# Kernel optimization log

Measured on AMD Instinct MI355X. Metric: run time of the kernel, lower is better.

Reference implementation:

```python
import jax, jax.numpy as jnp
import numpy as np

HEAD = 8
D = 128
GIN = 256
GOUT = 256
N = 50000
E = 800000


def gt_layer(edge_index, embeds, qT, kT, vT, ln_s, ln_b):
    rows, cols = edge_index[0], edge_index[1]
    n, d = embeds.shape
    hd = d // HEAD
    rowE = embeds[rows]  # [E, d]
    colE = embeds[cols]  # [E, d]
    q = (rowE @ qT).reshape(-1, HEAD, hd)
    k = (colE @ kT).reshape(-1, HEAD, hd)
    v = (colE @ vT).reshape(-1, HEAD, hd)
    att = jnp.clip(jnp.einsum('ehd,ehd->eh', q, k), -10.0, 10.0)
    expAtt = jnp.exp(att)  # [E, H]
    attNorm = jax.ops.segment_sum(expAtt, rows, num_segments=n)[rows]  # scatter-softmax denom
    att = expAtt / (attNorm + 1e-8)
    res = (att[..., None] * v).reshape(-1, d)  # [E, d]
    agg = jax.ops.segment_sum(res, rows, num_segments=n)  # [n, d]
    out = agg + embeds
    mu = jnp.mean(out, axis=-1, keepdims=True)
    var = jnp.mean((out - mu) ** 2, axis=-1, keepdims=True)
    return (out - mu) / jnp.sqrt(var + 1e-6) * ln_s + ln_b


def setup_inputs() -> dict:
    key = jax.random.key(0)
    ks = jax.random.split(key, 16)
    def xavier(k, shape):
        lim = np.sqrt(6.0 / (shape[0] + shape[1]))
        return jax.random.uniform(k, shape, jnp.float32, -lim, lim)
    inp = {
        'x': jax.random.normal(ks[0], (N, GIN), jnp.float32),
        'edge_index': jax.random.randint(ks[1], (2, E), 0, N, jnp.int64),
        'W_P_w': xavier(ks[2], (GIN, D)),
        'W_P_b': jnp.zeros((D,), jnp.float32),
        'W_pos': jax.random.uniform(ks[3], (1, D), jnp.float32, -0.02, 0.02),
        'q1': xavier(ks[4], (D, D)), 'k1': xavier(ks[5], (D, D)), 'v1': xavier(ks[6], (D, D)),
        'ln1_s': jnp.ones((D,), jnp.float32), 'ln1_b': jnp.zeros((D,), jnp.float32),
        'q2': xavier(ks[7], (D, D)), 'k2': xavier(ks[8], (D, D)), 'v2': xavier(ks[9], (D, D)),
        'ln2_s': jnp.ones((D,), jnp.float32), 'ln2_b': jnp.zeros((D,), jnp.float32),
        'inv_w': xavier(ks[10], (D, GOUT)),
        'inv_b': jnp.zeros((GOUT,), jnp.float32),
    }
    return inp


def reference(x, edge_index, W_P_w, W_P_b, W_pos, q1, k1, v1, ln1_s, ln1_b,
              q2, k2, v2, ln2_s, ln2_b, inv_w, inv_b):
    z = x @ W_P_w + W_P_b          # W_P linear: [N, D]
    embeds = z + W_pos              # if_pos; dropout is identity in eval
    embeds = gt_layer(edge_index, embeds, q1, k1, v1, ln1_s, ln1_b)
    embeds = gt_layer(edge_index, embeds, q2, k2, v2, ln2_s, ln2_b)
    return embeds @ inv_w + inv_b   # [N, GOUT]
```

## Files before the change

### kernel.cpp

```cpp
#include <hip/hip_runtime.h>
#include <hip/hip_bf16.h>

#define HEADS 8
#define DIM 128

typedef short s8v __attribute__((ext_vector_type(8)));
typedef float f4v __attribute__((ext_vector_type(4)));

__device__ __forceinline__ float bf2f(unsigned int lo16) {
    union { unsigned int i; float f; } v; v.i = lo16 << 16; return v.f;
}
__device__ __forceinline__ unsigned short f2bf(float f) {
    __hip_bfloat16 h = __float2bfloat16(f);
    return *reinterpret_cast<unsigned short*>(&h);
}
__device__ __forceinline__ int imin(int a, int b) { return a < b ? a : b; }

__global__ void detect_width_k(const unsigned int* __restrict__ w, int* __restrict__ flag) {
    __shared__ int cnt;
    if (threadIdx.x == 0) cnt = 0;
    __syncthreads();
    if (w[2 * threadIdx.x + 1] == 0u) atomicAdd(&cnt, 1);
    __syncthreads();
    if (threadIdx.x == 0) flag[0] = (cnt > 192) ? 1 : 0;
}

__global__ void cvt_edges_k(const void* __restrict__ ei, const int* __restrict__ flag,
                            int n2, int* __restrict__ out) {
    int i = blockIdx.x * 256 + threadIdx.x;
    if (i < n2) {
        if (flag[0])
            out[i] = (int)((const long long*)ei)[i];
        else
            out[i] = ((const int*)ei)[i];
    }
}

__global__ void count_deg_k(const int* __restrict__ rows, int E, int* __restrict__ deg) {
    int e = blockIdx.x * 256 + threadIdx.x;
    if (e < E) atomicAdd(&deg[rows[e]], 1);
}

__global__ void scan1_k(const int* __restrict__ deg, int n,
                        int* __restrict__ incl, int* __restrict__ blkSums) {
    __shared__ int s[256];
    int i = blockIdx.x * 256 + threadIdx.x;
    int v = (i < n) ? deg[i] : 0;
    s[threadIdx.x] = v;
    __syncthreads();
    for (int off = 1; off < 256; off <<= 1) {
        int t = (threadIdx.x >= off) ? s[threadIdx.x - off] : 0;
        __syncthreads();
        s[threadIdx.x] += t;
        __syncthreads();
    }
    if (i < n) incl[i] = s[threadIdx.x];
    if (threadIdx.x == 255) blkSums[blockIdx.x] = s[255];
}

__global__ void scan2_k(int* __restrict__ blkSums, int nb) {
    __shared__ int s[256];
    int v = (threadIdx.x < nb) ? blkSums[threadIdx.x] : 0;
    s[threadIdx.x] = v;
    __syncthreads();
    for (int off = 1; off < 256; off <<= 1) {
        int t = (threadIdx.x >= off) ? s[threadIdx.x - off] : 0;
        __syncthreads();
        s[threadIdx.x] += t;
        __syncthreads();
    }
    if (threadIdx.x < nb) blkSums[threadIdx.x] = s[threadIdx.x] - v;
}

__global__ void scan3_k(const int* __restrict__ incl, const int* __restrict__ deg,
                        const int* __restrict__ blkOff, int n,
                        int* __restrict__ rowPtr, int* __restrict__ cursor) {
    int i = blockIdx.x * 256 + threadIdx.x;
    if (i < n) {
        int inc = incl[i] + blkOff[blockIdx.x];
        rowPtr[i + 1] = inc;
        cursor[i] = inc - deg[i];
    }
    if (i == 0) rowPtr[0] = 0;
}

__global__ void scatter_k(const int* __restrict__ rows, const int* __restrict__ cols, int E,
                          int* __restrict__ cursor, int* __restrict__ colIdx) {
    int e = blockIdx.x * 256 + threadIdx.x;
    if (e < E) {
        int pos = atomicAdd(&cursor[rows[e]], 1);
        colIdx[pos] = cols[e];
    }
}

__global__ void build_wfrag_k(const float* __restrict__ W, unsigned short* __restrict__ dst,
                              int Kd, int Nd, int split, int ncomp) {
    int f = blockIdx.x * 256 + threadIdx.x;
    int KS = Kd >> 5;
    int perPhase = (Nd / 16 / split) * KS * 64;
    int total = ncomp * split * perPhase;
    if (f >= total) return;
    int comp = f / (split * perPhase);
    int r1 = f - comp * split * perPhase;
    int p = r1 / perPhase;
    int r = r1 - p * perPhase;
    int nt = r / (KS * 64);
    int r2 = r - nt * KS * 64;
    int ks = r2 >> 6, lane = r2 & 63;
    int n = p * (Nd / split) + nt * 16 + (lane & 15);
    int k0 = ks * 32 + (lane >> 4) * 8;
    unsigned short tmp[8];
#pragma unroll
    for (int j = 0; j < 8; j++) {
        float w = W[(size_t)(k0 + j) * Nd + n];
        unsigned short hi = f2bf(w);
        tmp[j] = (comp == 0) ? hi : f2bf(w - bf2f(hi));
    }
#pragma unroll
    for (int j = 0; j < 8; j++) dst[(size_t)f * 8 + j] = tmp[j];
}

__global__ __launch_bounds__(512) void proj_k(
    const float* __restrict__ A, const unsigned short* __restrict__ wfrag,
    const float* __restrict__ b0, const float* __restrict__ b1,
    unsigned short* __restrict__ ehi, unsigned short* __restrict__ elo, int M)
{
    constexpr int KD = 256, KS = 8, NTp = 4;
    constexpr int FRp = NTp * KS * 64;
    __shared__ s8v lds[2 * FRp];

    const int tid = threadIdx.x;
    const int lane = tid & 63;
    const int m16 = lane & 15, q4 = lane >> 4;
    const int phase = blockIdx.y;
    const int pairIdx = blockIdx.x * 8 + (tid >> 6);
    const int nPairs = (M + 31) >> 5;

    for (int idx = tid; idx < 2 * FRp; idx += 512) {
        int comp = idx / FRp, r = idx - comp * FRp;
        lds[idx] = *(const s8v*)(wfrag + ((size_t)((comp * 2 + phase) * FRp) + r) * 8);
    }
    __syncthreads();
    if (pairIdx >= nPairs) return;

    const int row0 = pairIdx * 32;
    const int rA0 = imin(row0 + m16, M - 1);
    const int rA1 = imin(row0 + 16 + m16, M - 1);

    f4v acc0[NTp], acc1[NTp];
#pragma unroll
    for (int nt = 0; nt < NTp; nt++) { acc0[nt] = (f4v){0,0,0,0}; acc1[nt] = (f4v){0,0,0,0}; }

    for (int ks = 0; ks < KS; ks++) {
        const float* pa0 = A + (size_t)rA0 * KD + ks * 32 + q4 * 8;
        const float* pa1 = A + (size_t)rA1 * KD + ks * 32 + q4 * 8;
        s8v a0h, a0l, a1h, a1l;
#pragma unroll
        for (int j = 0; j < 8; j++) {
            float x0 = pa0[j], x1 = pa1[j];
            unsigned short h0 = f2bf(x0), h1 = f2bf(x1);
            a0h[j] = (short)h0; a1h[j] = (short)h1;
            a0l[j] = (short)f2bf(x0 - bf2f(h0));
            a1l[j] = (short)f2bf(x1 - bf2f(h1));
        }
#pragma unroll
        for (int nt = 0; nt < NTp; nt++) {
            s8v bh = lds[0 * FRp + (nt * KS + ks) * 64 + lane];
            s8v bl = lds[1 * FRp + (nt * KS + ks) * 64 + lane];
            acc0[nt] = __builtin_amdgcn_mfma_f32_16x16x32_bf16(a0h, bh, acc0[nt], 0, 0, 0);
            acc0[nt] = __builtin_amdgcn_mfma_f32_16x16x32_bf16(a0h, bl, acc0[nt], 0, 0, 0);
            acc0[nt] = __builtin_amdgcn_mfma_f32_16x16x32_bf16(a0l, bh, acc0[nt], 0, 0, 0);
            acc1[nt] = __builtin_amdgcn_mfma_f32_16x16x32_bf16(a1h, bh, acc1[nt], 0, 0, 0);
            acc1[nt] = __builtin_amdgcn_mfma_f32_16x16x32_bf16(a1h, bl, acc1[nt], 0, 0, 0);
            acc1[nt] = __builtin_amdgcn_mfma_f32_16x16x32_bf16(a1l, bh, acc1[nt], 0, 0, 0);
        }
    }

#pragma unroll
    for (int nt = 0; nt < NTp; nt++) {
        const int col = phase * 64 + nt * 16 + m16;
        const float bias = b0[col] + b1[col];
#pragma unroll
        for (int r = 0; r < 4; r++) {
            const int gr0 = row0 + q4 * 4 + r;
            if (gr0 < M) {
                float v = acc0[nt][r] + bias;
                unsigned short h = f2bf(v);
                ehi[(size_t)gr0 * DIM + col] = h;
                elo[(size_t)gr0 * DIM + col] = f2bf(v - bf2f(h));
            }
            const int gr1 = gr0 + 16;
            if (gr1 < M && row0 + 16 < M) {
                float v = acc1[nt][r] + bias;
                unsigned short h = f2bf(v);
                ehi[(size_t)gr1 * DIM + col] = h;
                elo[(size_t)gr1 * DIM + col] = f2bf(v - bf2f(h));
            }
        }
    }
}

__global__ __launch_bounds__(512) void qkv_k(
    const unsigned short* __restrict__ ehi, const unsigned short* __restrict__ elo,
    const unsigned short* __restrict__ wfrag,
    float* __restrict__ Qb, unsigned short* __restrict__ KVb, int M)
{
    constexpr int KS = 4, NTp = 4;
    constexpr int FRp = NTp * KS * 64;
    constexpr int MATFR = 4 * FRp;
    __shared__ s8v lds[5 * FRp];

    const int tid = threadIdx.x;
    const int lane = tid & 63;
    const int m16 = lane & 15, q4 = lane >> 4;
    const int phase = blockIdx.y;
    const int pairIdx = blockIdx.x * 8 + (tid >> 6);
    const int nPairs = (M + 31) >> 5;

    for (int idx = tid; idx < 5 * FRp; idx += 512) {
        int s = idx / FRp, r = idx - s * FRp;
        int mat = (s < 2) ? 0 : (s < 4) ? 1 : 2;
        int comp = (s < 4) ? (s & 1) : 0;
        lds[idx] = *(const s8v*)(wfrag + ((size_t)mat * MATFR + (comp * 2 + phase) * FRp + r) * 8);
    }
    __syncthreads();
    if (pairIdx >= nPairs) return;

    const int row0 = pairIdx * 32;
    const int rA0 = imin(row0 + m16, M - 1);
    const int rA1 = imin(row0 + 16 + m16, M - 1);

    s8v a0h[KS], a0l[KS], a1h[KS], a1l[KS];
#pragma unroll
    for (int ks = 0; ks < KS; ks++) {
        a0h[ks] = *(const s8v*)(ehi + (size_t)rA0 * DIM + ks * 32 + q4 * 8);
        a0l[ks] = *(const s8v*)(elo + (size_t)rA0 * DIM + ks * 32 + q4 * 8);
        a1h[ks] = *(const s8v*)(ehi + (size_t)rA1 * DIM + ks * 32 + q4 * 8);
        a1l[ks] = *(const s8v*)(elo + (size_t)rA1 * DIM + ks * 32 + q4 * 8);
    }

    f4v aQ0[NTp], aQ1[NTp], aK0[NTp], aK1[NTp], aV0[NTp], aV1[NTp];
#pragma unroll
    for (int nt = 0; nt < NTp; nt++) {
        aQ0[nt] = (f4v){0,0,0,0}; aQ1[nt] = (f4v){0,0,0,0};
        aK0[nt] = (f4v){0,0,0,0}; aK1[nt] = (f4v){0,0,0,0};
        aV0[nt] = (f4v){0,0,0,0}; aV1[nt] = (f4v){0,0,0,0};
    }

#pragma unroll
    for (int ks = 0; ks < KS; ks++) {
#pragma unroll
        for (int nt = 0; nt < NTp; nt++) {
            const int fi = (nt * KS + ks) * 64 + lane;
            s8v qh = lds[0 * FRp + fi], ql = lds[1 * FRp + fi];
            s8v kh = lds[2 * FRp + fi], kl = lds[3 * FRp + fi];
            s8v vh = lds[4 * FRp + fi];
            aQ0[nt] = __builtin_amdgcn_mfma_f32_16x16x32_bf16(a0h[ks], qh, aQ0[nt], 0, 0, 0);
            aQ0[nt] = __builtin_amdgcn_mfma_f32_16x16x32_bf16(a0h[ks], ql, aQ0[nt], 0, 0, 0);
            aQ0[nt] = __builtin_amdgcn_mfma_f32_16x16x32_bf16(a0l[ks], qh, aQ0[nt], 0, 0, 0);
            aQ1[nt] = __builtin_amdgcn_mfma_f32_16x16x32_bf16(a1h[ks], qh, aQ1[nt], 0, 0, 0);
            aQ1[nt] = __builtin_amdgcn_mfma_f32_16x16x32_bf16(a1h[ks], ql, aQ1[nt], 0, 0, 0);
            aQ1[nt] = __builtin_amdgcn_mfma_f32_16x16x32_bf16(a1l[ks], qh, aQ1[nt], 0, 0, 0);
            aK0[nt] = __builtin_amdgcn_mfma_f32_16x16x32_bf16(a0h[ks], kh, aK0[nt], 0, 0, 0);
            aK0[nt] = __builtin_amdgcn_mfma_f32_16x16x32_bf16(a0h[ks], kl, aK0[nt], 0, 0, 0);
            aK0[nt] = __builtin_amdgcn_mfma_f32_16x16x32_bf16(a0l[ks], kh, aK0[nt], 0, 0, 0);
            aK1[nt] = __builtin_amdgcn_mfma_f32_16x16x32_bf16(a1h[ks], kh, aK1[nt], 0, 0, 0);
            aK1[nt] = __builtin_amdgcn_mfma_f32_16x16x32_bf16(a1h[ks], kl, aK1[nt], 0, 0, 0);
            aK1[nt] = __builtin_amdgcn_mfma_f32_16x16x32_bf16(a1l[ks], kh, aK1[nt], 0, 0, 0);
            aV0[nt] = __builtin_amdgcn_mfma_f32_16x16x32_bf16(a0h[ks], vh, aV0[nt], 0, 0, 0);
            aV0[nt] = __builtin_amdgcn_mfma_f32_16x16x32_bf16(a0l[ks], vh, aV0[nt], 0, 0, 0);
            aV1[nt] = __builtin_amdgcn_mfma_f32_16x16x32_bf16(a1h[ks], vh, aV1[nt], 0, 0, 0);
            aV1[nt] = __builtin_amdgcn_mfma_f32_16x16x32_bf16(a1l[ks], vh, aV1[nt], 0, 0, 0);
        }
    }

#pragma unroll
    for (int nt = 0; nt < NTp; nt++) {
        const int col = phase * 64 + nt * 16 + m16;
#pragma unroll
        for (int r = 0; r < 4; r++) {
            const int gr0 = row0 + q4 * 4 + r;
            if (gr0 < M) {
                Qb[(size_t)gr0 * DIM + col] = aQ0[nt][r];
                KVb[(size_t)gr0 * 256 + col] = f2bf(aK0[nt][r]);
                KVb[(size_t)gr0 * 256 + 128 + col] = f2bf(aV0[nt][r]);
            }
            const int gr1 = gr0 + 16;
            if (gr1 < M && row0 + 16 < M) {
                Qb[(size_t)gr1 * DIM + col] = aQ1[nt][r];
                KVb[(size_t)gr1 * 256 + col] = f2bf(aK1[nt][r]);
                KVb[(size_t)gr1 * 256 + 128 + col] = f2bf(aV1[nt][r]);
            }
        }
    }
}

__global__ __launch_bounds__(512) void outproj_k(
    const unsigned short* __restrict__ ehi, const unsigned short* __restrict__ elo,
    const unsigned short* __restrict__ wfrag, const float* __restrict__ b0,
    float* __restrict__ Out, int M)
{
    constexpr int KS = 4, NTp = 8, NOUT = 256;
    constexpr int FRp = NTp * KS * 64;
    __shared__ s8v lds[FRp];

    const int tid = threadIdx.x;
    const int lane = tid & 63;
    const int m16 = lane & 15, q4 = lane >> 4;
    const int phase = blockIdx.y;
    const int pairIdx = blockIdx.x * 8 + (tid >> 6);
    const int nPairs = (M + 31) >> 5;

    for (int idx = tid; idx < FRp; idx += 512)
        lds[idx] = *(const s8v*)(wfrag + ((size_t)phase * FRp + idx) * 8);
    __syncthreads();
    if (pairIdx >= nPairs) return;

    const int row0 = pairIdx * 32;
    const int rA0 = imin(row0 + m16, M - 1);
    const int rA1 = imin(row0 + 16 + m16, M - 1);

    s8v a0h[KS], a0l[KS], a1h[KS], a1l[KS];
#pragma unroll
    for (int ks = 0; ks < KS; ks++) {
        a0h[ks] = *(const s8v*)(ehi + (size_t)rA0 * DIM + ks * 32 + q4 * 8);
        a0l[ks] = *(const s8v*)(elo + (size_t)rA0 * DIM + ks * 32 + q4 * 8);
        a1h[ks] = *(const s8v*)(ehi + (size_t)rA1 * DIM + ks * 32 + q4 * 8);
        a1l[ks] = *(const s8v*)(elo + (size_t)rA1 * DIM + ks * 32 + q4 * 8);
    }

    f4v acc0[NTp], acc1[NTp];
#pragma unroll
    for (int nt = 0; nt < NTp; nt++) { acc0[nt] = (f4v){0,0,0,0}; acc1[nt] = (f4v){0,0,0,0}; }

#pragma unroll
    for (int ks = 0; ks < KS; ks++) {
#pragma unroll
        for (int nt = 0; nt < NTp; nt++) {
            s8v b = lds[(nt * KS + ks) * 64 + lane];
            acc0[nt] = __builtin_amdgcn_mfma_f32_16x16x32_bf16(a0h[ks], b, acc0[nt], 0, 0, 0);
            acc0[nt] = __builtin_amdgcn_mfma_f32_16x16x32_bf16(a0l[ks], b, acc0[nt], 0, 0, 0);
            acc1[nt] = __builtin_amdgcn_mfma_f32_16x16x32_bf16(a1h[ks], b, acc1[nt], 0, 0, 0);
            acc1[nt] = __builtin_amdgcn_mfma_f32_16x16x32_bf16(a1l[ks], b, acc1[nt], 0, 0, 0);
        }
    }

#pragma unroll
    for (int nt = 0; nt < NTp; nt++) {
        const int col = phase * 128 + nt * 16 + m16;
        const float bias = b0[col];
#pragma unroll
        for (int r = 0; r < 4; r++) {
            const int gr0 = row0 + q4 * 4 + r;
            if (gr0 < M) Out[(size_t)gr0 * NOUT + col] = acc0[nt][r] + bias;
            const int gr1 = gr0 + 16;
            if (gr1 < M && row0 + 16 < M) Out[(size_t)gr1 * NOUT + col] = acc1[nt][r] + bias;
        }
    }
}

__global__ __launch_bounds__(256) void agg_k(
    const float* __restrict__ Q, const unsigned short* __restrict__ KV,
    const int* __restrict__ rowPtr, const int* __restrict__ colIdx,
    const float* __restrict__ ln_s, const float* __restrict__ ln_b,
    unsigned short* __restrict__ ehi, unsigned short* __restrict__ elo, int n)
{
    const int node = blockIdx.x * 4 + (threadIdx.x >> 6);
    if (node >= n) return;
    const int lane = threadIdx.x & 63;
    const int d = lane * 2;

    const float2 q = *(const float2*)(Q + (size_t)node * DIM + d);
    const unsigned int rh = *(const unsigned int*)(ehi + (size_t)node * DIM + d);
    const unsigned int rl = *(const unsigned int*)(elo + (size_t)node * DIM + d);
    const float r0 = bf2f(rh & 0xffffu) + bf2f(rl & 0xffffu);
    const float r1 = bf2f(rh >> 16) + bf2f(rl >> 16);

    const int e0 = rowPtr[node], e1 = rowPtr[node + 1];
    float acc0 = 0.f, acc1 = 0.f, den = 0.f;

    if (e1 > e0) {
        int c = colIdx[e0];
        unsigned int ku = *(const unsigned int*)(KV + (size_t)c * 256 + d);
        unsigned int vu = *(const unsigned int*)(KV + (size_t)c * 256 + 128 + d);
        for (int e = e0; e < e1; e++) {
            unsigned int kuc = ku, vuc = vu;
            if (e + 1 < e1) {
                const int cn = colIdx[e + 1];
                ku = *(const unsigned int*)(KV + (size_t)cn * 256 + d);
                vu = *(const unsigned int*)(KV + (size_t)cn * 256 + 128 + d);
            }
            float p = q.x * bf2f(kuc & 0xffffu) + q.y * bf2f(kuc >> 16);
            p += __shfl_xor(p, 1);
            p += __shfl_xor(p, 2);
            p += __shfl_xor(p, 4);
            p = fminf(fmaxf(p, -10.f), 10.f);
            const float w = expf(p);
            den += w;
            acc0 += w * bf2f(vuc & 0xffffu);
            acc1 += w * bf2f(vuc >> 16);
        }
    }
    const float inv = 1.f / (den + 1e-8f);
    const float o0 = acc0 * inv + r0;
    const float o1 = acc1 * inv + r1;

    float s = o0 + o1, s2 = o0 * o0 + o1 * o1;
#pragma unroll
    for (int m = 1; m < 64; m <<= 1) {
        s  += __shfl_xor(s, m);
        s2 += __shfl_xor(s2, m);
    }
    const float mu = s * (1.f / 128.f);
    const float var = s2 * (1.f / 128.f) - mu * mu;
    const float rs = rsqrtf(var + 1e-6f);
    const float y0 = (o0 - mu) * rs * ln_s[d] + ln_b[d];
    const float y1 = (o1 - mu) * rs * ln_s[d + 1] + ln_b[d + 1];
    const unsigned short h0 = f2bf(y0), h1 = f2bf(y1);
    const unsigned short l0 = f2bf(y0 - bf2f(h0)), l1 = f2bf(y1 - bf2f(h1));
    *(unsigned int*)(ehi + (size_t)node * DIM + d) = (unsigned int)h0 | ((unsigned int)h1 << 16);
    *(unsigned int*)(elo + (size_t)node * DIM + d) = (unsigned int)l0 | ((unsigned int)l1 << 16);
}

extern "C" void kernel_launch(void* const* d_in, const int* in_sizes, int n_in,
                              void* d_out, int out_size, void* d_ws, size_t ws_size,
                              hipStream_t stream)
{
    const float* x    = (const float*)d_in[0];
    const void*  ei   = d_in[1];
    const float* Wp   = (const float*)d_in[2];
    const float* Wpb  = (const float*)d_in[3];
    const float* Wpos = (const float*)d_in[4];
    const float* q1   = (const float*)d_in[5];
    const float* k1   = (const float*)d_in[6];
    const float* v1   = (const float*)d_in[7];
    const float* l1s  = (const float*)d_in[8];
    const float* l1b  = (const float*)d_in[9];
    const float* q2   = (const float*)d_in[10];
    const float* k2   = (const float*)d_in[11];
    const float* v2   = (const float*)d_in[12];
    const float* l2s  = (const float*)d_in[13];
    const float* l2b  = (const float*)d_in[14];
    const float* invw = (const float*)d_in[15];
    const float* invb = (const float*)d_in[16];

    const int N = in_sizes[0] / 256;
    const int E = in_sizes[1] / 2;

    char* p = (char*)d_ws;
    auto carve = [&](size_t bytes) -> void* {
        void* r = (void*)p;
        p += (bytes + 255) & ~(size_t)255;
        return r;
    };
    unsigned short* ehi = (unsigned short*)carve((size_t)N * DIM * 2);
    unsigned short* elo = (unsigned short*)carve((size_t)N * DIM * 2);
    float*          Qb  = (float*)carve((size_t)N * DIM * 4);
    unsigned short* KVb = (unsigned short*)carve((size_t)N * 256 * 2);
    int*   deg    = (int*)carve((size_t)N * 4);
    int*   incl   = (int*)carve((size_t)N * 4);
    int*   blkS   = (int*)carve(1024);
    int*   rowPtr = (int*)carve((size_t)(N + 1) * 4);
    int*   cursor = (int*)carve((size_t)N * 4);
    int*   colIdx = (int*)carve((size_t)E * 4);
    int*   rc     = (int*)carve((size_t)2 * E * 4);
    int*   wflag  = (int*)carve(256);
    unsigned short* wfragP    = (unsigned short*)carve((size_t)2 * 256 * 128 * 2);
    unsigned short* wfragQKV1 = (unsigned short*)carve((size_t)3 * 2 * 128 * 128 * 2);
    unsigned short* wfragQKV2 = (unsigned short*)carve((size_t)3 * 2 * 128 * 128 * 2);
    unsigned short* wfragO    = (unsigned short*)carve((size_t)128 * 256 * 2);

    const size_t matStride = (size_t)2 * 128 * 128;

    int* rows = rc;
    int* cols = rc + E;

    const int nb  = (N + 255) / 256;
    const int ebl = (E + 255) / 256;
    const int nPairs = (N + 31) / 32;
    const dim3 ggrid((nPairs + 7) / 8, 2);

    detect_width_k<<<1, 256, 0, stream>>>((const unsigned int*)ei, wflag);
    cvt_edges_k<<<(2 * E + 255) / 256, 256, 0, stream>>>(ei, wflag, 2 * E, rc);
    hipMemsetAsync(deg, 0, (size_t)N * 4, stream);
    count_deg_k<<<ebl, 256, 0, stream>>>(rows, E, deg);
    scan1_k<<<nb, 256, 0, stream>>>(deg, N, incl, blkS);
    scan2_k<<<1, 256, 0, stream>>>(blkS, nb);
    scan3_k<<<nb, 256, 0, stream>>>(incl, deg, blkS, N, rowPtr, cursor);
    scatter_k<<<ebl, 256, 0, stream>>>(rows, cols, E, cursor, colIdx);

    build_wfrag_k<<<32, 256, 0, stream>>>(Wp, wfragP, 256, 128, 2, 2);
    build_wfrag_k<<<16, 256, 0, stream>>>(q1, wfragQKV1 + 0 * matStride, 128, 128, 2, 2);
    build_wfrag_k<<<16, 256, 0, stream>>>(k1, wfragQKV1 + 1 * matStride, 128, 128, 2, 2);
    build_wfrag_k<<<16, 256, 0, stream>>>(v1, wfragQKV1 + 2 * matStride, 128, 128, 2, 2);
    build_wfrag_k<<<16, 256, 0, stream>>>(q2, wfragQKV2 + 0 * matStride, 128, 128, 2, 2);
    build_wfrag_k<<<16, 256, 0, stream>>>(k2, wfragQKV2 + 1 * matStride, 128, 128, 2, 2);
    build_wfrag_k<<<16, 256, 0, stream>>>(v2, wfragQKV2 + 2 * matStride, 128, 128, 2, 2);
    build_wfrag_k<<<16, 256, 0, stream>>>(invw, wfragO, 128, 256, 2, 1);

    proj_k<<<ggrid, 512, 0, stream>>>(x, wfragP, Wpb, Wpos, ehi, elo, N);

    qkv_k<<<ggrid, 512, 0, stream>>>(ehi, elo, wfragQKV1, Qb, KVb, N);
    agg_k<<<(N + 3) / 4, 256, 0, stream>>>(Qb, KVb, rowPtr, colIdx, l1s, l1b, ehi, elo, N);

    qkv_k<<<ggrid, 512, 0, stream>>>(ehi, elo, wfragQKV2, Qb, KVb, N);
    agg_k<<<(N + 3) / 4, 256, 0, stream>>>(Qb, KVb, rowPtr, colIdx, l2s, l2b, ehi, elo, N);

    outproj_k<<<ggrid, 512, 0, stream>>>(ehi, elo, wfragO, invb, (float*)d_out, N);
}
```

Baseline: 552.5 us.

## Fuse setup kernels, read weights directly from global, batch edge gathers in aggregation

Merges width detection, edge conversion and degree counting into one kernel, and the eight weight-fragment builds into one launch. The GEMM kernels drop their LDS weight staging and read fragments straight from global (L2) with 256-thread blocks. proj_k uses vector loads for A. agg_k now prefetches four neighbour K/V rows at a time with double buffering and uses fast __expf. Together these cut launch overhead and expose more memory-level parallelism in the gather, at the cost of repeated global weight reads and slightly less precise exp.

```diff
diff --git a/kernel.cpp b/kernel.cpp
--- a/kernel.cpp
+++ b/kernel.cpp
@@ -16,29 +16,21 @@
 }
 __device__ __forceinline__ int imin(int a, int b) { return a < b ? a : b; }
 
-__global__ void detect_width_k(const unsigned int* __restrict__ w, int* __restrict__ flag) {
+__global__ __launch_bounds__(256) void setup_k(const void* __restrict__ ei, int n2, int E,
+                                               int* __restrict__ out, int* __restrict__ deg) {
     __shared__ int cnt;
+    const unsigned int* w = (const unsigned int*)ei;
     if (threadIdx.x == 0) cnt = 0;
     __syncthreads();
     if (w[2 * threadIdx.x + 1] == 0u) atomicAdd(&cnt, 1);
     __syncthreads();
-    if (threadIdx.x == 0) flag[0] = (cnt > 192) ? 1 : 0;
-}
-
-__global__ void cvt_edges_k(const void* __restrict__ ei, const int* __restrict__ flag,
-                            int n2, int* __restrict__ out) {
+    const bool is64 = cnt > 192;
     int i = blockIdx.x * 256 + threadIdx.x;
     if (i < n2) {
-        if (flag[0])
-            out[i] = (int)((const long long*)ei)[i];
-        else
-            out[i] = ((const int*)ei)[i];
-    }
-}
-
-__global__ void count_deg_k(const int* __restrict__ rows, int E, int* __restrict__ deg) {
-    int e = blockIdx.x * 256 + threadIdx.x;
-    if (e < E) atomicAdd(&deg[rows[e]], 1);
+        int v = is64 ? (int)((const long long*)ei)[i] : ((const int*)ei)[i];
+        out[i] = v;
+        if (i < E) atomicAdd(&deg[v], 1);
+    }
 }
 
 __global__ void scan1_k(const int* __restrict__ deg, int n,
@@ -93,13 +85,29 @@
     }
 }
 
-__global__ void build_wfrag_k(const float* __restrict__ W, unsigned short* __restrict__ dst,
-                              int Kd, int Nd, int split, int ncomp) {
-    int f = blockIdx.x * 256 + threadIdx.x;
+__global__ __launch_bounds__(256) void build_all_wfrag_k(
+    const float* __restrict__ Wp, const float* __restrict__ q1, const float* __restrict__ k1,
+    const float* __restrict__ v1, const float* __restrict__ q2, const float* __restrict__ k2,
+    const float* __restrict__ v2, const float* __restrict__ invw,
+    unsigned short* __restrict__ wfragP, unsigned short* __restrict__ wfragQKV1,
+    unsigned short* __restrict__ wfragQKV2, unsigned short* __restrict__ wfragO)
+{
+    const int b = blockIdx.x;
+    const float* W; unsigned short* dst; int Kd, Nd, ncomp, fb;
+    const int split = 2;
+    if (b < 32) { W = Wp; dst = wfragP; Kd = 256; Nd = 128; ncomp = 2; fb = b; }
+    else if (b < 128) {
+        int j = (b - 32) >> 4, r = (b - 32) & 15;
+        const float* ws[6] = { q1, k1, v1, q2, k2, v2 };
+        W = ws[j];
+        dst = ((j < 3) ? wfragQKV1 : wfragQKV2) + (size_t)(j % 3) * 2 * 128 * 128;
+        Kd = 128; Nd = 128; ncomp = 2; fb = r;
+    } else { W = invw; dst = wfragO; Kd = 128; Nd = 256; ncomp = 1; fb = b - 128; }
+
+    int f = fb * 256 + threadIdx.x;
     int KS = Kd >> 5;
     int perPhase = (Nd / 16 / split) * KS * 64;
-    int total = ncomp * split * perPhase;
-    if (f >= total) return;
+    if (f >= ncomp * split * perPhase) return;
     int comp = f / (split * perPhase);
     int r1 = f - comp * split * perPhase;
     int p = r1 / perPhase;
@@ -120,27 +128,18 @@
     for (int j = 0; j < 8; j++) dst[(size_t)f * 8 + j] = tmp[j];
 }
 
-__global__ __launch_bounds__(512) void proj_k(
+__global__ __launch_bounds__(256) void proj_k(
     const float* __restrict__ A, const unsigned short* __restrict__ wfrag,
     const float* __restrict__ b0, const float* __restrict__ b1,
     unsigned short* __restrict__ ehi, unsigned short* __restrict__ elo, int M)
 {
     constexpr int KD = 256, KS = 8, NTp = 4;
     constexpr int FRp = NTp * KS * 64;
-    __shared__ s8v lds[2 * FRp];
-
-    const int tid = threadIdx.x;
-    const int lane = tid & 63;
+    const int lane = threadIdx.x & 63;
     const int m16 = lane & 15, q4 = lane >> 4;
     const int phase = blockIdx.y;
-    const int pairIdx = blockIdx.x * 8 + (tid >> 6);
+    const int pairIdx = blockIdx.x * 4 + (threadIdx.x >> 6);
     const int nPairs = (M + 31) >> 5;
-
-    for (int idx = tid; idx < 2 * FRp; idx += 512) {
-        int comp = idx / FRp, r = idx - comp * FRp;
-        lds[idx] = *(const s8v*)(wfrag + ((size_t)((comp * 2 + phase) * FRp) + r) * 8);
-    }
-    __syncthreads();
     if (pairIdx >= nPairs) return;
 
     const int row0 = pairIdx * 32;
@@ -152,21 +151,23 @@
     for (int nt = 0; nt < NTp; nt++) { acc0[nt] = (f4v){0,0,0,0}; acc1[nt] = (f4v){0,0,0,0}; }
 
     for (int ks = 0; ks < KS; ks++) {
-        const float* pa0 = A + (size_t)rA0 * KD + ks * 32 + q4 * 8;
-        const float* pa1 = A + (size_t)rA1 * KD + ks * 32 + q4 * 8;
+        const f4v* pa0 = (const f4v*)(A + (size_t)rA0 * KD + ks * 32 + q4 * 8);
+        const f4v* pa1 = (const f4v*)(A + (size_t)rA1 * KD + ks * 32 + q4 * 8);
+        f4v xa = pa0[0], xb = pa0[1], ya = pa1[0], yb = pa1[1];
         s8v a0h, a0l, a1h, a1l;
 #pragma unroll
-        for (int j = 0; j < 8; j++) {
-            float x0 = pa0[j], x1 = pa1[j];
-            unsigned short h0 = f2bf(x0), h1 = f2bf(x1);
-            a0h[j] = (short)h0; a1h[j] = (short)h1;
-            a0l[j] = (short)f2bf(x0 - bf2f(h0));
-            a1l[j] = (short)f2bf(x1 - bf2f(h1));
+        for (int j = 0; j < 4; j++) {
+            unsigned short h;
+            h = f2bf(xa[j]); a0h[j] = (short)h; a0l[j] = (short)f2bf(xa[j] - bf2f(h));
+            h = f2bf(xb[j]); a0h[4 + j] = (short)h; a0l[4 + j] = (short)f2bf(xb[j] - bf2f(h));
+            h = f2bf(ya[j]); a1h[j] = (short)h; a1l[j] = (short)f2bf(ya[j] - bf2f(h));
+            h = f2bf(yb[j]); a1h[4 + j] = (short)h; a1l[4 + j] = (short)f2bf(yb[j] - bf2f(h));
         }
 #pragma unroll
         for (int nt = 0; nt < NTp; nt++) {
-            s8v bh = lds[0 * FRp + (nt * KS + ks) * 64 + lane];
-            s8v bl = lds[1 * FRp + (nt * KS + ks) * 64 + lane];
+            const size_t fi = ((size_t)(nt * KS + ks) * 64 + lane) * 8;
+            s8v bh = *(const s8v*)(wfrag + ((size_t)(0 * 2 + phase) * FRp) * 8 + fi);
+            s8v bl = *(const s8v*)(wfrag + ((size_t)(1 * 2 + phase) * FRp) * 8 + fi);
             acc0[nt] = __builtin_amdgcn_mfma_f32_16x16x32_bf16(a0h, bh, acc0[nt], 0, 0, 0);
             acc0[nt] = __builtin_amdgcn_mfma_f32_16x16x32_bf16(a0h, bl, acc0[nt], 0, 0, 0);
             acc0[nt] = __builtin_amdgcn_mfma_f32_16x16x32_bf16(a0l, bh, acc0[nt], 0, 0, 0);
@@ -200,7 +201,7 @@
     }
 }
 
-__global__ __launch_bounds__(512) void qkv_k(
+__global__ __launch_bounds__(256) void qkv_k(
     const unsigned short* __restrict__ ehi, const unsigned short* __restrict__ elo,
     const unsigned short* __restrict__ wfrag,
     float* __restrict__ Qb, unsigned short* __restrict__ KVb, int M)
@@ -208,22 +209,11 @@
     constexpr int KS = 4, NTp = 4;
     constexpr int FRp = NTp * KS * 64;
     constexpr int MATFR = 4 * FRp;
-    __shared__ s8v lds[5 * FRp];
-
-    const int tid = threadIdx.x;
-    const int lane = tid & 63;
+    const int lane = threadIdx.x & 63;
     const int m16 = lane & 15, q4 = lane >> 4;
     const int phase = blockIdx.y;
-    const int pairIdx = blockIdx.x * 8 + (tid >> 6);
+    const int pairIdx = blockIdx.x * 4 + (threadIdx.x >> 6);
     const int nPairs = (M + 31) >> 5;
-
-    for (int idx = tid; idx < 5 * FRp; idx += 512) {
-        int s = idx / FRp, r = idx - s * FRp;
-        int mat = (s < 2) ? 0 : (s < 4) ? 1 : 2;
-        int comp = (s < 4) ? (s & 1) : 0;
-        lds[idx] = *(const s8v*)(wfrag + ((size_t)mat * MATFR + (comp * 2 + phase) * FRp + r) * 8);
-    }
-    __syncthreads();
     if (pairIdx >= nPairs) return;
 
     const int row0 = pairIdx * 32;
@@ -251,10 +241,12 @@
     for (int ks = 0; ks < KS; ks++) {
 #pragma unroll
         for (int nt = 0; nt < NTp; nt++) {
-            const int fi = (nt * KS + ks) * 64 + lane;
-            s8v qh = lds[0 * FRp + fi], ql = lds[1 * FRp + fi];
-            s8v kh = lds[2 * FRp + fi], kl = lds[3 * FRp + fi];
-            s8v vh = lds[4 * FRp + fi];
+            const size_t fi = ((size_t)(nt * KS + ks) * 64 + lane) * 8;
+            s8v qh = *(const s8v*)(wfrag + (size_t)(0 * MATFR + (0 * 2 + phase) * FRp) * 8 + fi);
+            s8v ql = *(const s8v*)(wfrag + (size_t)(0 * MATFR + (1 * 2 + phase) * FRp) * 8 + fi);
+            s8v kh = *(const s8v*)(wfrag + (size_t)(1 * MATFR + (0 * 2 + phase) * FRp) * 8 + fi);
+            s8v kl = *(const s8v*)(wfrag + (size_t)(1 * MATFR + (1 * 2 + phase) * FRp) * 8 + fi);
+            s8v vh = *(const s8v*)(wfrag + (size_t)(2 * MATFR + (0 * 2 + phase) * FRp) * 8 + fi);
             aQ0[nt] = __builtin_amdgcn_mfma_f32_16x16x32_bf16(a0h[ks], qh, aQ0[nt], 0, 0, 0);
             aQ0[nt] = __builtin_amdgcn_mfma_f32_16x16x32_bf16(a0h[ks], ql, aQ0[nt], 0, 0, 0);
             aQ0[nt] = __builtin_amdgcn_mfma_f32_16x16x32_bf16(a0l[ks], qh, aQ0[nt], 0, 0, 0);
@@ -295,25 +287,18 @@
     }
 }
 
-__global__ __launch_bounds__(512) void outproj_k(
+__global__ __launch_bounds__(256) void outproj_k(
     const unsigned short* __restrict__ ehi, const unsigned short* __restrict__ elo,
     const unsigned short* __restrict__ wfrag, const float* __restrict__ b0,
     float* __restrict__ Out, int M)
 {
     constexpr int KS = 4, NTp = 8, NOUT = 256;
     constexpr int FRp = NTp * KS * 64;
-    __shared__ s8v lds[FRp];
-
-    const int tid = threadIdx.x;
-    const int lane = tid & 63;
+    const int lane = threadIdx.x & 63;
     const int m16 = lane & 15, q4 = lane >> 4;
     const int phase = blockIdx.y;
-    const int pairIdx = blockIdx.x * 8 + (tid >> 6);
+    const int pairIdx = blockIdx.x * 4 + (threadIdx.x >> 6);
     const int nPairs = (M + 31) >> 5;
-
-    for (int idx = tid; idx < FRp; idx += 512)
-        lds[idx] = *(const s8v*)(wfrag + ((size_t)phase * FRp + idx) * 8);
-    __syncthreads();
     if (pairIdx >= nPairs) return;
 
     const int row0 = pairIdx * 32;
@@ -337,7 +322,7 @@
     for (int ks = 0; ks < KS; ks++) {
 #pragma unroll
         for (int nt = 0; nt < NTp; nt++) {
-            s8v b = lds[(nt * KS + ks) * 64 + lane];
+            s8v b = *(const s8v*)(wfrag + ((size_t)phase * FRp + (size_t)(nt * KS + ks) * 64 + lane) * 8);
             acc0[nt] = __builtin_amdgcn_mfma_f32_16x16x32_bf16(a0h[ks], b, acc0[nt], 0, 0, 0);
             acc0[nt] = __builtin_amdgcn_mfma_f32_16x16x32_bf16(a0l[ks], b, acc0[nt], 0, 0, 0);
             acc1[nt] = __builtin_amdgcn_mfma_f32_16x16x32_bf16(a1h[ks], b, acc1[nt], 0, 0, 0);
@@ -380,26 +365,51 @@
     float acc0 = 0.f, acc1 = 0.f, den = 0.f;
 
     if (e1 > e0) {
-        int c = colIdx[e0];
-        unsigned int ku = *(const unsigned int*)(KV + (size_t)c * 256 + d);
-        unsigned int vu = *(const unsigned int*)(KV + (size_t)c * 256 + 128 + d);
-        for (int e = e0; e < e1; e++) {
-            unsigned int kuc = ku, vuc = vu;
-            if (e + 1 < e1) {
-                const int cn = colIdx[e + 1];
-                ku = *(const unsigned int*)(KV + (size_t)cn * 256 + d);
-                vu = *(const unsigned int*)(KV + (size_t)cn * 256 + 128 + d);
-            }
-            float p = q.x * bf2f(kuc & 0xffffu) + q.y * bf2f(kuc >> 16);
-            p += __shfl_xor(p, 1);
-            p += __shfl_xor(p, 2);
-            p += __shfl_xor(p, 4);
-            p = fminf(fmaxf(p, -10.f), 10.f);
-            const float w = expf(p);
-            den += w;
-            acc0 += w * bf2f(vuc & 0xffffu);
-            acc1 += w * bf2f(vuc >> 16);
-        }
+        unsigned int kA[4], vA[4], kB[4], vB[4];
+#define LOADC(karr, varr, base_)                                        \
+        {                                                               \
+            _Pragma("unroll")                                           \
+            for (int j = 0; j < 4; j++) {                               \
+                int idx = (base_) + j;                                  \
+                int cc = colIdx[idx < e1 ? idx : e1 - 1];               \
+                size_t off = (size_t)cc * 256 + d;                      \
+                karr[j] = *(const unsigned int*)(KV + off);             \
+                varr[j] = *(const unsigned int*)(KV + off + 128);       \
+            }                                                           \
+        }
+#define COMP(karr, varr, base_)                                         \
+        {                                                               \
+            _Pragma("unroll")                                           \
+            for (int j = 0; j < 4; j++) {                               \
+                if ((base_) + j < e1) {                                 \
+                    float p = q.x * bf2f(karr[j] & 0xffffu)             \
+                            + q.y * bf2f(karr[j] >> 16);                \
+                    p += __shfl_xor(p, 1);                              \
+                    p += __shfl_xor(p, 2);                              \
+                    p += __shfl_xor(p, 4);                              \
+                    p = fminf(fmaxf(p, -10.f), 10.f);                   \
+                    float w = __expf(p);                                \
+                    den += w;                                           \
+                    acc0 += w * bf2f(varr[j] & 0xffffu);                \
+                    acc1 += w * bf2f(varr[j] >> 16);                    \
+                }                                                       \
+            }                                                           \
+        }
+        int base = e0;
+        LOADC(kA, vA, base)
+        while (base < e1) {
+            int nxt = base + 4;
+            if (nxt < e1) LOADC(kB, vB, nxt)
+            COMP(kA, vA, base)
+            base = nxt;
+            if (base >= e1) break;
+            int nxt2 = base + 4;
+            if (nxt2 < e1) LOADC(kA, vA, nxt2)
+            COMP(kB, vB, base)
+            base = nxt2;
+        }
+#undef LOADC
+#undef COMP
     }
     const float inv = 1.f / (den + 1e-8f);
     const float o0 = acc0 * inv + r0;
@@ -464,47 +474,36 @@
     int*   cursor = (int*)carve((size_t)N * 4);
     int*   colIdx = (int*)carve((size_t)E * 4);
     int*   rc     = (int*)carve((size_t)2 * E * 4);
-    int*   wflag  = (int*)carve(256);
     unsigned short* wfragP    = (unsigned short*)carve((size_t)2 * 256 * 128 * 2);
     unsigned short* wfragQKV1 = (unsigned short*)carve((size_t)3 * 2 * 128 * 128 * 2);
     unsigned short* wfragQKV2 = (unsigned short*)carve((size_t)3 * 2 * 128 * 128 * 2);
     unsigned short* wfragO    = (unsigned short*)carve((size_t)128 * 256 * 2);
 
-    const size_t matStride = (size_t)2 * 128 * 128;
-
     int* rows = rc;
     int* cols = rc + E;
 
     const int nb  = (N + 255) / 256;
     const int ebl = (E + 255) / 256;
     const int nPairs = (N + 31) / 32;
-    const dim3 ggrid((nPairs + 7) / 8, 2);
-
-    detect_width_k<<<1, 256, 0, stream>>>((const unsigned int*)ei, wflag);
-    cvt_edges_k<<<(2 * E + 255) / 256, 256, 0, stream>>>(ei, wflag, 2 * E, rc);
+    const dim3 ggrid((nPairs + 3) / 4, 2);
+
     hipMemsetAsync(deg, 0, (size_t)N * 4, stream);
-    count_deg_k<<<ebl, 256, 0, stream>>>(rows, E, deg);
+    setup_k<<<(2 * E + 255) / 256, 256, 0, stream>>>(ei, 2 * E, E, rc, deg);
     scan1_k<<<nb, 256, 0, stream>>>(deg, N, incl, blkS);
     scan2_k<<<1, 256, 0, stream>>>(blkS, nb);
     scan3_k<<<nb, 256, 0, stream>>>(incl, deg, blkS, N, rowPtr, cursor);
     scatter_k<<<ebl, 256, 0, stream>>>(rows, cols, E, cursor, colIdx);
 
-    build_wfrag_k<<<32, 256, 0, stream>>>(Wp, wfragP, 256, 128, 2, 2);
-    build_wfrag_k<<<16, 256, 0, stream>>>(q1, wfragQKV1 + 0 * matStride, 128, 128, 2, 2);
-    build_wfrag_k<<<16, 256, 0, stream>>>(k1, wfragQKV1 + 1 * matStride, 128, 128, 2, 2);
-    build_wfrag_k<<<16, 256, 0, stream>>>(v1, wfragQKV1 + 2 * matStride, 128, 128, 2, 2);
-    build_wfrag_k<<<16, 256, 0, stream>>>(q2, wfragQKV2 + 0 * matStride, 128, 128, 2, 2);
-    build_wfrag_k<<<16, 256, 0, stream>>>(k2, wfragQKV2 + 1 * matStride, 128, 128, 2, 2);
-    build_wfrag_k<<<16, 256, 0, stream>>>(v2, wfragQKV2 + 2 * matStride, 128, 128, 2, 2);
-    build_wfrag_k<<<16, 256, 0, stream>>>(invw, wfragO, 128, 256, 2, 1);
-
-    proj_k<<<ggrid, 512, 0, stream>>>(x, wfragP, Wpb, Wpos, ehi, elo, N);
-
-    qkv_k<<<ggrid, 512, 0, stream>>>(ehi, elo, wfragQKV1, Qb, KVb, N);
+    build_all_wfrag_k<<<144, 256, 0, stream>>>(Wp, q1, k1, v1, q2, k2, v2, invw,
+                                               wfragP, wfragQKV1, wfragQKV2, wfragO);
+
+    proj_k<<<ggrid, 256, 0, stream>>>(x, wfragP, Wpb, Wpos, ehi, elo, N);
+
+    qkv_k<<<ggrid, 256, 0, stream>>>(ehi, elo, wfragQKV1, Qb, KVb, N);
     agg_k<<<(N + 3) / 4, 256, 0, stream>>>(Qb, KVb, rowPtr, colIdx, l1s, l1b, ehi, elo, N);
 
-    qkv_k<<<ggrid, 512, 0, stream>>>(ehi, elo, wfragQKV2, Qb, KVb, N);
+    qkv_k<<<ggrid, 256, 0, stream>>>(ehi, elo, wfragQKV2, Qb, KVb, N);
     agg_k<<<(N + 3) / 4, 256, 0, stream>>>(Qb, KVb, rowPtr, colIdx, l2s, l2b, ehi, elo, N);
 
-    outproj_k<<<ggrid, 512, 0, stream>>>(ehi, elo, wfragO, invb, (float*)d_out, N);
-}
+    outproj_k<<<ggrid, 256, 0, stream>>>(ehi, elo, wfragO, invb, (float*)d_out, N);
+}
```

After: 502.0 us. -9.1%, faster.
